# Kernel tuning notes

Measured on AMD Instinct MI355X. Metric: run time of the kernel, lower is better.

Reference implementation:

```python
import jax, jax.numpy as jnp
import numpy as np

WAY, SHOT, P, FDIM, HDIM, NHEADS = 5, 5, 10, 640, 512, 8
H = W = 14
NUM_SPT = WAY * SHOT
EPS_BN = 1e-5
EPS_LN = 1e-5


def _l2norm(x, axis=-1):
    n = jnp.linalg.norm(x, axis=axis, keepdims=True)
    return x / jnp.maximum(n, 1e-12)


def _cbr(x, Wc, bc, g, beta):
    # 1x1 conv + BatchNorm(train stats) + ReLU. x: [N,C,H,W], Wc: [O,C]
    y = jnp.einsum('nchw,oc->nohw', x, Wc) + bc[None, :, None, None]
    mu = y.mean((0, 2, 3))
    var = y.var((0, 2, 3))
    y = (y - mu[None, :, None, None]) / jnp.sqrt(var[None, :, None, None] + EPS_BN)
    y = y * g[None, :, None, None] + beta[None, :, None, None]
    return jax.nn.relu(y)


def _mha(x, Wq, bq, Wk, bk, Wv, bv, Wa, ba, ln_g, ln_b):
    B, S, D = x.shape
    dk = D // NHEADS
    def proj(Wt, bt):
        return (x @ Wt.T + bt).reshape(B, S, NHEADS, dk).transpose(0, 2, 1, 3)
    q, k, v = proj(Wq, bq), proj(Wk, bk), proj(Wv, bv)
    scores = jnp.einsum('bhqd,bhkd->bhqk', q, k) / jnp.sqrt(jnp.asarray(dk, x.dtype))
    att = jax.nn.softmax(scores, axis=-1)
    ctx = jnp.einsum('bhqk,bhkd->bhqd', att, v).transpose(0, 2, 1, 3).reshape(B, S, D)
    out = ctx @ Wa.T + ba + x  # residual
    mu = out.mean(-1, keepdims=True)
    var = out.var(-1, keepdims=True)
    return ((out - mu) / jnp.sqrt(var + EPS_LN)) * ln_g + ln_b


def setup_inputs() -> dict:
    k = jax.random.key(0)
    ks = jax.random.split(k, 16)
    s = 0.02
    return {
        'key':   jax.random.normal(ks[0], (NUM_SPT + 75, FDIM, H, W), jnp.float32),
        'query': jax.random.normal(ks[1], (75, FDIM, H, W), jnp.float32),
        'Wc':  jax.random.normal(ks[2], (HDIM, FDIM), jnp.float32) * s,
        'bc':  jnp.zeros((HDIM,), jnp.float32),
        'g1':  jnp.ones((HDIM,), jnp.float32),
        'b1':  jnp.zeros((HDIM,), jnp.float32),
        'Wq':  jax.random.normal(ks[3], (HDIM, HDIM), jnp.float32) * s,
        'bq':  jnp.zeros((HDIM,), jnp.float32),
        'Wk':  jax.random.normal(ks[4], (HDIM, HDIM), jnp.float32) * s,
        'bk':  jnp.zeros((HDIM,), jnp.float32),
        'Wv':  jax.random.normal(ks[5], (HDIM, HDIM), jnp.float32) * s,
        'bv':  jnp.zeros((HDIM,), jnp.float32),
        'Wa':  jax.random.normal(ks[6], (HDIM, HDIM), jnp.float32) * s,
        'ba':  jnp.zeros((HDIM,), jnp.float32),
        'ln_g': jnp.ones((HDIM,), jnp.float32),
        'ln_b': jnp.zeros((HDIM,), jnp.float32),
        'Wm':  jax.random.normal(ks[7], (P, HDIM), jnp.float32) * s,
        'Wo':  jax.random.normal(ks[8], (FDIM, HDIM), jnp.float32) * s,
        'bo':  jnp.zeros((FDIM,), jnp.float32),
        'g2':  jnp.ones((FDIM,), jnp.float32),
        'b2':  jnp.zeros((FDIM,), jnp.float32),
    }


def reference(key, query, Wc, bc, g1, b1, Wq, bq, Wk, bk, Wv, bv, Wa, ba, ln_g, ln_b, Wm, Wo, bo, g2, b2):
    # proto_concept: conv1x1 + BN + ReLU
    key_ = _cbr(key, Wc, bc, g1, b1)                 # [B, HDIM, H, W]
    B, D, h, w = key_.shape
    feats = key_.transpose(0, 2, 3, 1).reshape(B, h * w, D)
    support = feats[:NUM_SPT].reshape(SHOT, WAY, h * w, D).mean(0)   # [WAY, hw, D]
    qf = feats[NUM_SPT:]                                             # [NQ, hw, D]
    nq = B - NUM_SPT

    support = _mha(support, Wq, bq, Wk, bk, Wv, bv, Wa, ba, ln_g, ln_b)
    qf = _mha(qf, Wq, bq, Wk, bk, Wv, bv, Wa, ba, ln_g, ln_b)

    # prototype formation: softmax over all support positions (dim 0)
    mw = (support @ Wm.T).reshape(-1, P, 1)          # [WAY*hw, P, 1]
    mw = jax.nn.softmax(mw, axis=0)
    sflat = support.reshape(-1, D)                   # [WAY*hw, D]
    protos = (mw * sflat[:, None, :]).sum(0)         # [P, D]

    # ---- query_loss (training branch) ----
    protos_n = _l2norm(protos)                       # [P, D]

    # diversity loss (faithful to original incl. triu over (P, D) dims)
    diff2 = (protos_n[None, :, :] - protos_n[:, None, :]) ** 2   # [P, P, D]
    dis = 1.0 - diff2[None]                                      # [1, P, P, D]
    dis = dis * (dis > 0).astype(dis.dtype)
    tri = jnp.triu(jnp.ones((P, D), dis.dtype), k=1)
    dis = dis * tri
    dis_loss = (dis.sum(1).sum(1) * 2.0 / (P * (P - 1))).mean()

    cst_loss = ((protos_n[1:] - protos_n[:-1]) ** 2).sum(-1).mean()

    # dual-softmax scoring (protos shared across batch)
    score = jnp.einsum('bnd,md->bnm', qf, protos_n)  # [NQ, hw, P]
    sp = jax.nn.softmax(score, axis=-1)
    new_q = _l2norm(jnp.einsum('bnm,md->bnd', sp, protos_n))

    idx = jnp.argmax(score, axis=-1)                 # top-1 proto per position
    pos = protos_n[idx]                              # [NQ, hw, D]
    fea_loss = jnp.mean((qf - pos) ** 2)

    uq = new_q.transpose(0, 2, 1).reshape(nq, D, h, w)
    updated = _cbr(uq, Wo, bo, g2, b2) + query       # [NQ, FDIM, H, W]
    return (updated, fea_loss, cst_loss, dis_loss)
```

## Files before the change

kernel.cpp:

```cpp
#include <hip/hip_runtime.h>
#include <math.h>

#define WAYS 5
#define SHOTS 5
#define PP 10
#define FDIMC 640
#define HD 512
#define SEQ 196
#define NB 100
#define NQB 75
#define NMHA 80
#define M1 (NB*SEQ)
#define MMHA (NMHA*SEQ)
#define MQ (NQB*SEQ)
#define NBLK_ROWK (MQ/4)
#define OUT_UPD (NQB*FDIMC*SEQ)

#define OFF_CS1S 0
#define OFF_CS1Q 512
#define OFF_CS2S 1024
#define OFF_CS2Q 1664
#define ZERO_FLOATS 2306
#define OFF_ST1SC 2308
#define OFF_ST1SH 2820
#define OFF_ST2SC 3332
#define OFF_ST2SH 3972
#define OFF_M    4612
#define OFF_PN   14412

#define RB 20480
#define RC (RB + 15439360)
#define RD (RC + 8028160)
#define RE (RD + 8028160)
#define RF (RE + 8028160)
#define RG (RF + 4014080)
#define RH (RG + 4014080)
#define OFF_FEAP (RF + 3763200)
#define OFF_WSM  RB
#define OFF_PPART (RB + 16384)

typedef __bf16 bf16x8 __attribute__((ext_vector_type(8)));
typedef float f32x4 __attribute__((ext_vector_type(4)));

__device__ __forceinline__ ushort f2bf(float f) {
  unsigned u = __float_as_uint(f);
  return (ushort)((u + 0x7fffu + ((u >> 16) & 1u)) >> 16);
}

__device__ __forceinline__ f32x4 mfma16(bf16x8 a, bf16x8 b, f32x4 c) {
  return __builtin_amdgcn_mfma_f32_16x16x32_bf16(a, b, c, 0, 0, 0);
}

__device__ __forceinline__ float waveSum(float v) {
#pragma unroll
  for (int o = 32; o; o >>= 1) v += __shfl_xor(v, o, 64);
  return v;
}


__global__ __launch_bounds__(256) void key_transpose(const float* __restrict__ key,
                                                     ushort* __restrict__ keyT) {
  __shared__ float T[32][33];
  const int n = blockIdx.z, c0 = blockIdx.y*32, s0 = blockIdx.x*32;
  const int tj = threadIdx.x & 31, ti = threadIdx.x >> 5;
#pragma unroll
  for (int it = 0; it < 4; ++it) {
    const int cl = it*8 + ti;
    const int s = s0 + tj;
    T[cl][tj] = (s < SEQ) ? key[((size_t)n*FDIMC + c0 + cl)*SEQ + s] : 0.f;
  }
  __syncthreads();
#pragma unroll
  for (int it = 0; it < 4; ++it) {
    const int sl = it*8 + ti;
    const int s = s0 + sl;
    if (s < SEQ) keyT[((size_t)(n*SEQ + s))*FDIMC + c0 + tj] = f2bf(T[tj][sl]);
  }
}

__global__ void wconvert(const float* __restrict__ Wc, const float* __restrict__ Wq,
                         const float* __restrict__ Wk, const float* __restrict__ Wv,
                         const float* __restrict__ Wa, const float* __restrict__ Wo,
                         ushort* __restrict__ wh) {
  const int i = blockIdx.x*256 + threadIdx.x;
  float v;
  if (i < 327680) v = Wc[i];
  else if (i < 589824) v = Wq[i - 327680];
  else if (i < 851968) v = Wk[i - 589824];
  else if (i < 1114112) v = Wv[i - 851968];
  else if (i < 1376256) v = Wa[i - 1114112];
  else v = Wo[i - 1376256];
  wh[i] = f2bf(v);
}

template<int OM, int CS>
__global__ __launch_bounds__(256) void gemm_bf(const ushort* __restrict__ A,
    const ushort* __restrict__ W, const float* __restrict__ bias,
    float* __restrict__ Cf, ushort* __restrict__ Ch, int M, int N, int K,
    float* __restrict__ gsum, float* __restrict__ gsq) {
  __shared__ ushort As[128*32];
  __shared__ ushort Bs[128*32];
  __shared__ float csum[128], csq[128];
  const int tid = threadIdx.x;
  const int m0 = blockIdx.y*128, n0 = blockIdx.x*128;
  const int w = tid >> 6, lane = tid & 63;
  const int wr = w >> 1, wc = w & 1;
  const int g = lane >> 4, c = lane & 15;

  const int ch0 = tid, ch1 = 256 + tid;
  const int ar0 = ch0 >> 2, ar1 = ch1 >> 2;
  const int ak0 = (ch0 & 3) * 8, ak1 = (ch1 & 3) * 8;
  int gr0 = m0 + ar0; if (gr0 > M-1) gr0 = M-1;
  int gr1 = m0 + ar1; if (gr1 > M-1) gr1 = M-1;
  const ushort* Ap0 = A + (size_t)gr0*K + ak0;
  const ushort* Ap1 = A + (size_t)gr1*K + ak1;
  const ushort* Wp0 = W + (size_t)(n0 + ar0)*K + ak0;
  const ushort* Wp1 = W + (size_t)(n0 + ar1)*K + ak1;

  f32x4 acc[4][4];
#pragma unroll
  for (int i = 0; i < 4; ++i)
#pragma unroll
    for (int j = 0; j < 4; ++j) acc[i][j] = (f32x4)(0.0f);

  for (int k0 = 0; k0 < K; k0 += 32) {
    const uint4 a0 = *(const uint4*)(Ap0 + k0);
    const uint4 a1 = *(const uint4*)(Ap1 + k0);
    const uint4 b0 = *(const uint4*)(Wp0 + k0);
    const uint4 b1 = *(const uint4*)(Wp1 + k0);
    __syncthreads();
    *(uint4*)(&As[ch0*8]) = a0;
    *(uint4*)(&As[ch1*8]) = a1;
    *(uint4*)(&Bs[ch0*8]) = b0;
    *(uint4*)(&Bs[ch1*8]) = b1;
    __syncthreads();
    bf16x8 af[4], bfr[4];
#pragma unroll
    for (int mi = 0; mi < 4; ++mi)
      af[mi] = *(const bf16x8*)(&As[(wr*64 + mi*16 + c)*32 + g*8]);
#pragma unroll
    for (int ni = 0; ni < 4; ++ni)
      bfr[ni] = *(const bf16x8*)(&Bs[(wc*64 + ni*16 + c)*32 + g*8]);
#pragma unroll
    for (int mi = 0; mi < 4; ++mi)
#pragma unroll
      for (int ni = 0; ni < 4; ++ni)
        acc[mi][ni] = mfma16(af[mi], bfr[ni], acc[mi][ni]);
  }

  if (CS) {
    __syncthreads();
    if (tid < 128) { csum[tid] = 0.f; csq[tid] = 0.f; }
    __syncthreads();
  }

#pragma unroll
  for (int ni = 0; ni < 4; ++ni) {
    const int col = n0 + wc*64 + ni*16 + c;
    const float bb = bias[col];
    float ls = 0.f, lq = 0.f;
#pragma unroll
    for (int mi = 0; mi < 4; ++mi) {
#pragma unroll
      for (int q = 0; q < 4; ++q) {
        const int row = m0 + wr*64 + mi*16 + g*4 + q;
        if (row < M) {
          const float v = acc[mi][ni][q] + bb;
          if (OM == 0) Cf[(size_t)row*N + col] = v;
          else if (OM == 1) Ch[(size_t)row*N + col] = f2bf(v);
          else Ch[(size_t)row*N + col] = f2bf(v*0.125f);
          if (CS) { ls += v; lq += v*v; }
        }
      }
    }
    if (CS) {
      const int lcol = wc*64 + ni*16 + c;
      atomicAdd(&csum[lcol], ls);
      atomicAdd(&csq[lcol], lq);
    }
  }
  if (CS) {
    __syncthreads();
    if (tid < 128) {
      atomicAdd(&gsum[n0 + tid], csum[tid]);
      atomicAdd(&gsq[n0 + tid], csq[tid]);
    }
  }
}


__global__ void bn_finalize(const float* __restrict__ sums, const float* __restrict__ sumsq,
    const float* __restrict__ g, const float* __restrict__ b, int C, float invM,
    float* __restrict__ scale, float* __restrict__ shift) {
  const int c = blockIdx.x*256 + threadIdx.x;
  if (c >= C) return;
  const float mu = sums[c]*invM;
  const float var = sumsq[c]*invM - mu*mu;
  const float sc = rsqrtf(var + 1e-5f) * g[c];
  scale[c] = sc;
  shift[c] = b[c] - mu*sc;
}

__global__ __launch_bounds__(256) void bn1_apply(const float* __restrict__ y1,
    const float* __restrict__ scale, const float* __restrict__ shift,
    float* __restrict__ sraw, float* __restrict__ xbuf, ushort* __restrict__ xbufh) {
  const int i4 = blockIdx.x*256 + threadIdx.x;
  if (i4 >= M1*HD/4) return;
  const int e = i4 << 2;
  const int col = e & (HD - 1);
  float4 v = ((const float4*)y1)[i4];
  v.x = fmaxf(fmaf(v.x, scale[col],   shift[col]),   0.f);
  v.y = fmaxf(fmaf(v.y, scale[col+1], shift[col+1]), 0.f);
  v.z = fmaxf(fmaf(v.z, scale[col+2], shift[col+2]), 0.f);
  v.w = fmaxf(fmaf(v.w, scale[col+3], shift[col+3]), 0.f);
  if (e < 25*SEQ*HD) ((float4*)sraw)[i4] = v;
  else {
    const int o4 = i4 - (20*SEQ*HD/4);
    ((float4*)xbuf)[o4] = v;
    ushort4 hv = make_ushort4(f2bf(v.x), f2bf(v.y), f2bf(v.z), f2bf(v.w));
    *(ushort4*)(xbufh + (size_t)o4*4) = hv;
  }
}

__global__ void support_mean(const float* __restrict__ sraw, float* __restrict__ xbuf,
                             ushort* __restrict__ xbufh) {
  const int i4 = blockIdx.x*256 + threadIdx.x;
  if (i4 >= WAYS*SEQ*HD/4) return;
  const int e = i4 << 2;
  const int w = e / (SEQ*HD);
  const int rem = e - w*(SEQ*HD);
  float4 acc = make_float4(0.f,0.f,0.f,0.f);
#pragma unroll
  for (int s = 0; s < SHOTS; ++s) {
    const float4 v = *(const float4*)(sraw + (s*WAYS + w)*(SEQ*HD) + rem);
    acc.x += v.x; acc.y += v.y; acc.z += v.z; acc.w += v.w;
  }
  acc.x *= 0.2f; acc.y *= 0.2f; acc.z *= 0.2f; acc.w *= 0.2f;
  ((float4*)xbuf)[i4] = acc;
  ushort4 hv = make_ushort4(f2bf(acc.x), f2bf(acc.y), f2bf(acc.z), f2bf(acc.w));
  *(ushort4*)(xbufh + (size_t)i4*4) = hv;
}


__global__ __launch_bounds__(256) void attn_qk(const ushort* __restrict__ qb,
    const ushort* __restrict__ kb, ushort* __restrict__ P) {
  __shared__ ushort Ks[208*72];
  const int bh = blockIdx.x, b = bh >> 3, h = bh & 7;
  const int tid = threadIdx.x;
  for (int idx = tid; idx < 208*8; idx += 256) {
    const int row = idx >> 3, part = idx & 7;
    uint4 v = make_uint4(0u,0u,0u,0u);
    if (row < SEQ) v = *(const uint4*)(kb + ((size_t)(b*SEQ + row))*HD + h*64 + part*8);
    *(uint4*)(&Ks[row*72 + part*8]) = v;
  }
  __syncthreads();
  const int w = tid >> 6, lane = tid & 63, g = lane >> 4, c = lane & 15;
  for (int rt = w; rt < 13; rt += 4) {
    int qrow = b*SEQ + rt*16 + c; if (qrow > MMHA-1) qrow = MMHA-1;
    const bf16x8 aq0 = *(const bf16x8*)(qb + (size_t)qrow*HD + h*64 + g*8);
    const bf16x8 aq1 = *(const bf16x8*)(qb + (size_t)qrow*HD + h*64 + 32 + g*8);
    f32x4 acc[13];
#pragma unroll
    for (int ct = 0; ct < 13; ++ct) acc[ct] = (f32x4)(0.0f);
#pragma unroll
    for (int ct = 0; ct < 13; ++ct) {
      const bf16x8 b0 = *(const bf16x8*)(&Ks[(ct*16 + c)*72 + g*8]);
      const bf16x8 b1 = *(const bf16x8*)(&Ks[(ct*16 + c)*72 + 32 + g*8]);
      acc[ct] = mfma16(aq0, b0, acc[ct]);
      acc[ct] = mfma16(aq1, b1, acc[ct]);
    }
    if (c >= 4) acc[12] = (f32x4)(-1e30f);
    float mrow[4], Z[4];
#pragma unroll
    for (int q = 0; q < 4; ++q) {
      float mx = acc[0][q];
#pragma unroll
      for (int ct = 1; ct < 13; ++ct) mx = fmaxf(mx, acc[ct][q]);
      mrow[q] = mx;
    }
#pragma unroll
    for (int q = 0; q < 4; ++q) {
#pragma unroll
      for (int msk = 1; msk < 16; msk <<= 1)
        mrow[q] = fmaxf(mrow[q], __shfl_xor(mrow[q], msk, 64));
    }
#pragma unroll
    for (int q = 0; q < 4; ++q) Z[q] = 0.f;
#pragma unroll
    for (int ct = 0; ct < 13; ++ct)
#pragma unroll
      for (int q = 0; q < 4; ++q) {
        const float e = __expf(acc[ct][q] - mrow[q]);
        acc[ct][q] = e; Z[q] += e;
      }
#pragma unroll
    for (int q = 0; q < 4; ++q) {
#pragma unroll
      for (int msk = 1; msk < 16; msk <<= 1) Z[q] += __shfl_xor(Z[q], msk, 64);
      Z[q] = 1.f / Z[q];
    }
    const size_t pb = (size_t)bh*(208*232);
#pragma unroll
    for (int q = 0; q < 4; ++q) {
      ushort* pr = P + pb + (size_t)(rt*16 + g*4 + q)*232;
#pragma unroll
      for (int ct = 0; ct < 13; ++ct) pr[ct*16 + c] = f2bf(acc[ct][q]*Z[q]);
      pr[208 + c] = 0;
      if (c < 8) pr[224 + c] = 0;
    }
  }
}


__global__ __launch_bounds__(256) void v_transpose(const ushort* __restrict__ vb,
                                                   ushort* __restrict__ VT) {
  __shared__ ushort Vs[196*72];
  const int bh = blockIdx.x, b = bh >> 3, h = bh & 7;
  const int tid = threadIdx.x;
  for (int idx = tid; idx < 196*8; idx += 256) {
    const int row = idx >> 3, part = idx & 7;
    *(uint4*)(&Vs[row*72 + part*8]) =
        *(const uint4*)(vb + ((size_t)(b*SEQ + row))*HD + h*64 + part*8);
  }
  __syncthreads();
  ushort* o = VT + (size_t)bh*64*224;
  for (int idx = tid; idx < 64*224; idx += 256) {
    const int d = idx/224, s = idx - d*224;
    o[idx] = (s < SEQ) ? Vs[s*72 + d] : (ushort)0;
  }
}


__global__ __launch_bounds__(256) void attn_pv(const ushort* __restrict__ P,
    const ushort* __restrict__ VT, ushort* __restrict__ ctx) {
  __shared__ ushort Ps[112*232];
  const int bh = blockIdx.x, b = bh >> 3, h = bh & 7;
  const int tid = threadIdx.x, w = tid >> 6, lane = tid & 63, g = lane >> 4, c = lane & 15;
  bf16x8 bv[7];
  const ushort* vt = VT + (size_t)bh*64*224 + (size_t)(w*16 + c)*224;
#pragma unroll
  for (int ks = 0; ks < 7; ++ks) bv[ks] = *(const bf16x8*)(vt + ks*32 + g*8);
  const char* pg = (const char*)(P + (size_t)bh*(208*232));
#pragma unroll
  for (int half = 0; half < 2; ++half) {
    const int r0 = half ? 112 : 0;
    const int nbytes = half ? 96*464 : 112*464;
    __syncthreads();
    for (int byte = tid*16; byte < nbytes; byte += 4096)
      *(uint4*)((char*)Ps + byte) = *(const uint4*)(pg + r0*464 + byte);
    __syncthreads();
    const int rtlo = half ? 7 : 0, rthi = half ? 13 : 7;
    for (int rt = rtlo; rt < rthi; ++rt) {
      const int lrow = rt*16 - r0 + c;
      f32x4 acc = (f32x4)(0.0f);
#pragma unroll
      for (int ks = 0; ks < 7; ++ks) {
        const bf16x8 a = *(const bf16x8*)(&Ps[lrow*232 + ks*32 + g*8]);
        acc = mfma16(a, bv[ks], acc);
      }
#pragma unroll
      for (int q = 0; q < 4; ++q) {
        const int srow = rt*16 + g*4 + q;
        if (srow < SEQ)
          ctx[((size_t)(b*SEQ + srow))*HD + h*64 + w*16 + c] = f2bf(acc[q]);
      }
    }
  }
}


__global__ __launch_bounds__(256) void ln_kernel(const float* __restrict__ tmp,
    const float* __restrict__ xin, const float* __restrict__ g,
    const float* __restrict__ bta, float* __restrict__ out) {
  const int row = blockIdx.x*4 + (threadIdx.x >> 6);
  const int lane = threadIdx.x & 63;
  const float* t = tmp + (size_t)row*HD;
  const float* x = xin + (size_t)row*HD;
  float v[8]; float s = 0.f;
#pragma unroll
  for (int i = 0; i < 8; ++i) { const float val = t[i*64 + lane] + x[i*64 + lane]; v[i] = val; s += val; }
  s = waveSum(s);
  const float mu = s * (1.f/HD);
  float sq = 0.f;
#pragma unroll
  for (int i = 0; i < 8; ++i) { const float d = v[i] - mu; sq += d*d; }
  sq = waveSum(sq);
  const float istd = rsqrtf(sq*(1.f/HD) + 1e-5f);
#pragma unroll
  for (int i = 0; i < 8; ++i) {
    const int d = i*64 + lane;
    out[(size_t)row*HD + d] = (v[i] - mu)*istd*g[d] + bta[d];
  }
}


__global__ __launch_bounds__(256) void mw_kernel(const float* __restrict__ xout,
    const float* __restrict__ Wm, float* __restrict__ m) {
  const int row = blockIdx.x*4 + (threadIdx.x >> 6);
  const int lane = threadIdx.x & 63;
  const float* x = xout + (size_t)row*HD;
  float xv[8];
#pragma unroll
  for (int i = 0; i < 8; ++i) xv[i] = x[i*64 + lane];
#pragma unroll
  for (int p = 0; p < PP; ++p) {
    const float* wp = Wm + p*HD;
    float s = 0.f;
#pragma unroll
    for (int i = 0; i < 8; ++i) s = fmaf(xv[i], wp[i*64 + lane], s);
    s = waveSum(s);
    if (lane == 0) m[row*PP + p] = s;
  }
}

__global__ __launch_bounds__(256) void wsm_kernel(const float* __restrict__ m,
                                                  float* __restrict__ wsm) {
  __shared__ float red[256];
  const int p = blockIdx.x, tid = threadIdx.x;
  float lmax = -1e30f;
  for (int r = tid; r < 980; r += 256) lmax = fmaxf(lmax, m[r*PP + p]);
  red[tid] = lmax; __syncthreads();
  for (int s = 128; s; s >>= 1) { if (tid < s) red[tid] = fmaxf(red[tid], red[tid+s]); __syncthreads(); }
  const float bmax = red[0]; __syncthreads();
  float lsum = 0.f;
  for (int r = tid; r < 980; r += 256) {
    const float e = __expf(m[r*PP + p] - bmax);
    wsm[p*980 + r] = e; lsum += e;
  }
  red[tid] = lsum; __syncthreads();
  for (int s = 128; s; s >>= 1) { if (tid < s) red[tid] += red[tid+s]; __syncthreads(); }
  const float invZ = 1.f / red[0];
  for (int r = tid; r < 980; r += 256) wsm[p*980 + r] *= invZ;
}

__global__ __launch_bounds__(256) void protos_part(const float* __restrict__ wsm,
    const float* __restrict__ xout, float* __restrict__ part) {
  const int p = blockIdx.y, chunk = blockIdx.x, tid = threadIdx.x;
  const int r0 = chunk*49;
  float a0 = 0.f, a1 = 0.f;
  for (int r = r0; r < r0 + 49; ++r) {
    const float w = wsm[p*980 + r];
    a0 = fmaf(w, xout[(size_t)r*HD + tid], a0);
    a1 = fmaf(w, xout[(size_t)r*HD + tid + 256], a1);
  }
  float* o = part + (((size_t)p*20 + chunk) << 9);
  o[tid] = a0;
  o[tid + 256] = a1;
}

__global__ __launch_bounds__(256) void protos_fin(const float* __restrict__ part,
                                                  float* __restrict__ pn) {
  __shared__ float red[256];
  const int p = blockIdx.x, tid = threadIdx.x;
  float a0 = 0.f, a1 = 0.f;
  for (int cch = 0; cch < 20; ++cch) {
    const float* o = part + (((size_t)p*20 + cch) << 9);
    a0 += o[tid];
    a1 += o[tid + 256];
  }
  red[tid] = a0*a0 + a1*a1; __syncthreads();
  for (int s = 128; s; s >>= 1) { if (tid < s) red[tid] += red[tid+s]; __syncthreads(); }
  const float rn = 1.f / fmaxf(sqrtf(red[0]), 1e-12f);
  pn[p*HD + tid] = a0*rn;
  pn[p*HD + tid + 256] = a1*rn;
}

__global__ __launch_bounds__(256) void losses_kernel(const float* __restrict__ pn, float* __restrict__ out) {
  __shared__ float redc[256], redd[256];
  const int tid = threadIdx.x;
  float cpart = 0.f, dpart = 0.f;
  for (int d = tid; d < HD; d += 256) {
    float a[PP];
#pragma unroll
    for (int j = 0; j < PP; ++j) a[j] = pn[j*HD + d];
#pragma unroll
    for (int j = 0; j < PP; ++j) {
      if (d > j) {
#pragma unroll
        for (int i = 0; i < PP; ++i) {
          const float df = a[j] - a[i];
          const float t = 1.f - df*df;
          if (t > 0.f) dpart += t;
        }
      }
    }
#pragma unroll
    for (int j = 0; j < PP - 1; ++j) { const float df = a[j+1] - a[j]; cpart += df*df; }
  }
  redc[tid] = cpart; redd[tid] = dpart; __syncthreads();
  for (int s = 128; s; s >>= 1) {
    if (tid < s) { redc[tid] += redc[tid+s]; redd[tid] += redd[tid+s]; }
    __syncthreads();
  }
  if (tid == 0) {
    out[OUT_UPD + 1] = redc[0] / 9.f;
    out[OUT_UPD + 2] = redd[0] * (2.f / (90.f * 512.f));
  }
}

__global__ __launch_bounds__(256) void rowk(const float* __restrict__ xout, const float* __restrict__ pn,
    ushort* __restrict__ newq, float* __restrict__ feapart) {
  __shared__ float Ps[PP*HD];
  __shared__ float fred[4];
  const int tid = threadIdx.x;
  for (int idx = tid; idx < PP*HD; idx += 256) Ps[idx] = pn[idx];
  __syncthreads();
  const int row = blockIdx.x*4 + (tid >> 6);
  const int lane = tid & 63;
  const float* x = xout + (size_t)(WAYS*SEQ + row)*HD;
  float xv[8];
#pragma unroll
  for (int i = 0; i < 8; ++i) xv[i] = x[i*64 + lane];
  float sc[PP];
#pragma unroll
  for (int p = 0; p < PP; ++p) {
    float s = 0.f;
#pragma unroll
    for (int i = 0; i < 8; ++i) s = fmaf(xv[i], Ps[p*HD + i*64 + lane], s);
    sc[p] = waveSum(s);
  }
  float mx = sc[0]; int am = 0;
#pragma unroll
  for (int p = 1; p < PP; ++p) if (sc[p] > mx) { mx = sc[p]; am = p; }
  float Z = 0.f; float sp[PP];
#pragma unroll
  for (int p = 0; p < PP; ++p) { const float e = expf(sc[p] - mx); sp[p] = e; Z += e; }
  const float rz = 1.f / Z;
  float nv[8]; float ss = 0.f;
#pragma unroll
  for (int i = 0; i < 8; ++i) {
    float a = 0.f;
#pragma unroll
    for (int p = 0; p < PP; ++p) a = fmaf(sp[p], Ps[p*HD + i*64 + lane], a);
    a *= rz; nv[i] = a; ss += a*a;
  }
  ss = waveSum(ss);
  const float rn = 1.f / fmaxf(sqrtf(ss), 1e-12f);
#pragma unroll
  for (int i = 0; i < 8; ++i) newq[(size_t)row*HD + i*64 + lane] = f2bf(nv[i]*rn);
  float fp = 0.f;
#pragma unroll
  for (int i = 0; i < 8; ++i) { const float d = xv[i] - Ps[am*HD + i*64 + lane]; fp += d*d; }
  fp = waveSum(fp);
  if (lane == 0) fred[tid >> 6] = fp;
  __syncthreads();
  if (tid == 0) feapart[blockIdx.x] = fred[0] + fred[1] + fred[2] + fred[3];
}

__global__ __launch_bounds__(256) void fea_finalize(const float* __restrict__ feapart,
                                                    float* __restrict__ out) {
  __shared__ float red[256];
  float s = 0.f;
  for (int i = threadIdx.x; i < NBLK_ROWK; i += 256) s += feapart[i];
  red[threadIdx.x] = s; __syncthreads();
  for (int st = 128; st; st >>= 1) {
    if (threadIdx.x < st) red[threadIdx.x] += red[threadIdx.x + st];
    __syncthreads();
  }
  if (threadIdx.x == 0) out[OUT_UPD] = red[0] / (float)((size_t)NQB*SEQ*HD);
}

__global__ __launch_bounds__(256) void bn2_apply(const float* __restrict__ y2, const float* __restrict__ scale,
    const float* __restrict__ shift, const float* __restrict__ query, float* __restrict__ out) {
  __shared__ float tile[32][33];
  const int n = blockIdx.z, o0 = blockIdx.y*32, hw0 = blockIdx.x*32;
  const int tj = threadIdx.x & 31, ti = threadIdx.x >> 5;
#pragma unroll
  for (int it = 0; it < 4; ++it) {
    const int hw = hw0 + it*8 + ti;
    const int o = o0 + tj;
    float v = 0.f;
    if (hw < SEQ) v = fmaxf(fmaf(y2[((size_t)n*SEQ + hw)*FDIMC + o], scale[o], shift[o]), 0.f);
    tile[it*8 + ti][tj] = v;
  }
  __syncthreads();
#pragma unroll
  for (int it = 0; it < 4; ++it) {
    const int o = o0 + it*8 + ti;
    const int hw = hw0 + tj;
    if (hw < SEQ) {
      const size_t oi = ((size_t)n*FDIMC + o)*SEQ + hw;
      out[oi] = tile[tj][it*8 + ti] + query[oi];
    }
  }
}

extern "C" void kernel_launch(void* const* d_in, const int* in_sizes, int n_in,
                              void* d_out, int out_size, void* d_ws, size_t ws_size,
                              hipStream_t stream) {
  const float* key   = (const float*)d_in[0];
  const float* query = (const float*)d_in[1];
  const float* Wc    = (const float*)d_in[2];
  const float* bc    = (const float*)d_in[3];
  const float* g1    = (const float*)d_in[4];
  const float* b1    = (const float*)d_in[5];
  const float* Wq    = (const float*)d_in[6];
  const float* bq    = (const float*)d_in[7];
  const float* Wk    = (const float*)d_in[8];
  const float* bk    = (const float*)d_in[9];
  const float* Wv    = (const float*)d_in[10];
  const float* bv    = (const float*)d_in[11];
  const float* Wa    = (const float*)d_in[12];
  const float* ba    = (const float*)d_in[13];
  const float* ln_g  = (const float*)d_in[14];
  const float* ln_b  = (const float*)d_in[15];
  const float* Wm    = (const float*)d_in[16];
  const float* Wo    = (const float*)d_in[17];
  const float* bo    = (const float*)d_in[18];
  const float* g2    = (const float*)d_in[19];
  const float* b2    = (const float*)d_in[20];
  float* out = (float*)d_out;
  float* w = (float*)d_ws;

  float*  y1    = w + RB;
  ushort* P     = (ushort*)(w + RB);
  float*  y2    = w + RB;
  float*  xbuf  = w + RC;
  ushort* keyT  = (ushort*)(w + RD);
  ushort* qb    = (ushort*)(w + RD);
  float*  tmp   = w + RD;
  ushort* xbufh = (ushort*)(w + RE);
  ushort* VT    = (ushort*)(w + RE);
  float*  xout  = w + RE;
  float*  sraw  = w + RF;
  ushort* kb    = (ushort*)(w + RF);
  ushort* newq  = (ushort*)(w + RF);
  ushort* vb    = (ushort*)(w + RG);
  ushort* ctx   = (ushort*)(w + RG);
  ushort* wh    = (ushort*)(w + RH);
  float*  feapart = w + OFF_FEAP;
  float*  wsm   = w + OFF_WSM;
  float*  ppart = w + OFF_PPART;
  ushort* Wcb = wh;
  ushort* Wqb = wh + 327680;
  ushort* Wkb = wh + 589824;
  ushort* Wvb = wh + 851968;
  ushort* Wab = wh + 1114112;
  ushort* Wob = wh + 1376256;

  hipMemsetAsync(w, 0, ZERO_FLOATS*sizeof(float), stream);

  key_transpose<<<dim3(7, 20, NB), 256, 0, stream>>>(key, keyT);
  wconvert<<<6656, 256, 0, stream>>>(Wc, Wq, Wk, Wv, Wa, Wo, wh);

  gemm_bf<0,1><<<dim3(4, 154), 256, 0, stream>>>(keyT, Wcb, bc, y1, nullptr, M1, HD, FDIMC,
                                                 w + OFF_CS1S, w + OFF_CS1Q);
  bn_finalize<<<2, 256, 0, stream>>>(w + OFF_CS1S, w + OFF_CS1Q, g1, b1, HD, 1.f/M1,
                                     w + OFF_ST1SC, w + OFF_ST1SH);
  bn1_apply<<<M1*HD/4/256, 256, 0, stream>>>(y1, w + OFF_ST1SC, w + OFF_ST1SH, sraw, xbuf, xbufh);
  support_mean<<<WAYS*SEQ*HD/4/256, 256, 0, stream>>>(sraw, xbuf, xbufh);

  gemm_bf<2,0><<<dim3(4, 123), 256, 0, stream>>>(xbufh, Wqb, bq, nullptr, qb, MMHA, HD, HD, nullptr, nullptr);
  gemm_bf<1,0><<<dim3(4, 123), 256, 0, stream>>>(xbufh, Wkb, bk, nullptr, kb, MMHA, HD, HD, nullptr, nullptr);
  gemm_bf<1,0><<<dim3(4, 123), 256, 0, stream>>>(xbufh, Wvb, bv, nullptr, vb, MMHA, HD, HD, nullptr, nullptr);

  v_transpose<<<NMHA*8, 256, 0, stream>>>(vb, VT);
  attn_qk<<<NMHA*8, 256, 0, stream>>>(qb, kb, P);
  attn_pv<<<NMHA*8, 256, 0, stream>>>(P, VT, ctx);

  gemm_bf<0,0><<<dim3(4, 123), 256, 0, stream>>>(ctx, Wab, ba, tmp, nullptr, MMHA, HD, HD, nullptr, nullptr);
  ln_kernel<<<MMHA/4, 256, 0, stream>>>(tmp, xbuf, ln_g, ln_b, xout);

  mw_kernel<<<245, 256, 0, stream>>>(xout, Wm, w + OFF_M);
  wsm_kernel<<<PP, 256, 0, stream>>>(w + OFF_M, wsm);
  protos_part<<<dim3(20, PP), 256, 0, stream>>>(wsm, xout, ppart);
  protos_fin<<<PP, 256, 0, stream>>>(ppart, w + OFF_PN);
  losses_kernel<<<1, 256, 0, stream>>>(w + OFF_PN, out);
  rowk<<<NBLK_ROWK, 256, 0, stream>>>(xout, w + OFF_PN, newq, feapart);

  gemm_bf<0,1><<<dim3(5, 115), 256, 0, stream>>>(newq, Wob, bo, y2, nullptr, MQ, FDIMC, HD,
                                                 w + OFF_CS2S, w + OFF_CS2Q);
  bn_finalize<<<3, 256, 0, stream>>>(w + OFF_CS2S, w + OFF_CS2Q, g2, b2, FDIMC, 1.f/MQ,
                                     w + OFF_ST2SC, w + OFF_ST2SH);
  fea_finalize<<<1, 256, 0, stream>>>(feapart, out);
  bn2_apply<<<dim3(7, 20, NQB), 256, 0, stream>>>(y2, w + OFF_ST2SC, w + OFF_ST2SH, query, out);
}
```

Before: 393.0 us.

## Store conv1 output and intermediate activations in bf16 instead of fp32

The first conv GEMM now writes bf16, and bn1_apply, support_mean, ln_kernel and the downstream proto/rowk kernels read and write bf16 activations instead of fp32 copies. The fp32 xbuf/sraw/xout buffers are dropped, and workspace regions are remapped so the new buffers do not collide. This roughly halves the memory traffic of these bandwidth-bound elementwise kernels. In exchange it adds bf16 rounding to the residual input of the layer norm and to the proto computation.

```diff
diff --git a/kernel.cpp b/kernel.cpp
--- a/kernel.cpp
+++ b/kernel.cpp
@@ -35,9 +35,10 @@
 #define RF (RE + 8028160)
 #define RG (RF + 4014080)
 #define RH (RG + 4014080)
+#define OFF_XOUT (RB + 10000000)
 #define OFF_FEAP (RF + 3763200)
-#define OFF_WSM  RB
-#define OFF_PPART (RB + 16384)
+#define OFF_WSM  RG
+#define OFF_PPART (RG + 16384)
 
 typedef __bf16 bf16x8 __attribute__((ext_vector_type(8)));
 typedef float f32x4 __attribute__((ext_vector_type(4)));
@@ -45,6 +46,9 @@
 __device__ __forceinline__ ushort f2bf(float f) {
   unsigned u = __float_as_uint(f);
   return (ushort)((u + 0x7fffu + ((u >> 16) & 1u)) >> 16);
+}
+__device__ __forceinline__ float bf2f(ushort u) {
+  return __uint_as_float(((unsigned)u) << 16);
 }
 
 __device__ __forceinline__ f32x4 mfma16(bf16x8 a, bf16x8 b, f32x4 c) {
@@ -201,44 +205,51 @@
   shift[c] = b[c] - mu*sc;
 }
 
-__global__ __launch_bounds__(256) void bn1_apply(const float* __restrict__ y1,
+__global__ __launch_bounds__(256) void bn1_apply(const ushort* __restrict__ y1,
     const float* __restrict__ scale, const float* __restrict__ shift,
-    float* __restrict__ sraw, float* __restrict__ xbuf, ushort* __restrict__ xbufh) {
-  const int i4 = blockIdx.x*256 + threadIdx.x;
-  if (i4 >= M1*HD/4) return;
-  const int e = i4 << 2;
+    ushort* __restrict__ srawh, ushort* __restrict__ xbufh) {
+  const int i8 = blockIdx.x*256 + threadIdx.x;
+  if (i8 >= M1*HD/8) return;
+  const int e = i8 << 3;
   const int col = e & (HD - 1);
-  float4 v = ((const float4*)y1)[i4];
-  v.x = fmaxf(fmaf(v.x, scale[col],   shift[col]),   0.f);
-  v.y = fmaxf(fmaf(v.y, scale[col+1], shift[col+1]), 0.f);
-  v.z = fmaxf(fmaf(v.z, scale[col+2], shift[col+2]), 0.f);
-  v.w = fmaxf(fmaf(v.w, scale[col+3], shift[col+3]), 0.f);
-  if (e < 25*SEQ*HD) ((float4*)sraw)[i4] = v;
-  else {
-    const int o4 = i4 - (20*SEQ*HD/4);
-    ((float4*)xbuf)[o4] = v;
-    ushort4 hv = make_ushort4(f2bf(v.x), f2bf(v.y), f2bf(v.z), f2bf(v.w));
-    *(ushort4*)(xbufh + (size_t)o4*4) = hv;
-  }
-}
-
-__global__ void support_mean(const float* __restrict__ sraw, float* __restrict__ xbuf,
-                             ushort* __restrict__ xbufh) {
-  const int i4 = blockIdx.x*256 + threadIdx.x;
-  if (i4 >= WAYS*SEQ*HD/4) return;
-  const int e = i4 << 2;
+  const uint4 raw = ((const uint4*)y1)[i8];
+  unsigned rw[4] = {raw.x, raw.y, raw.z, raw.w};
+  unsigned res[4];
+#pragma unroll
+  for (int j = 0; j < 4; ++j) {
+    float v0 = bf2f((ushort)(rw[j] & 0xffffu));
+    float v1 = bf2f((ushort)(rw[j] >> 16));
+    v0 = fmaxf(fmaf(v0, scale[col + 2*j],     shift[col + 2*j]),     0.f);
+    v1 = fmaxf(fmaf(v1, scale[col + 2*j + 1], shift[col + 2*j + 1]), 0.f);
+    res[j] = (unsigned)f2bf(v0) | ((unsigned)f2bf(v1) << 16);
+  }
+  const uint4 o = make_uint4(res[0], res[1], res[2], res[3]);
+  if (e < 25*SEQ*HD) ((uint4*)srawh)[i8] = o;
+  else ((uint4*)xbufh)[i8 - (20*SEQ*HD/8)] = o;
+}
+
+__global__ void support_mean(const ushort* __restrict__ srawh, ushort* __restrict__ xbufh) {
+  const int i8 = blockIdx.x*256 + threadIdx.x;
+  if (i8 >= WAYS*SEQ*HD/8) return;
+  const int e = i8 << 3;
   const int w = e / (SEQ*HD);
   const int rem = e - w*(SEQ*HD);
-  float4 acc = make_float4(0.f,0.f,0.f,0.f);
+  float acc[8] = {};
 #pragma unroll
   for (int s = 0; s < SHOTS; ++s) {
-    const float4 v = *(const float4*)(sraw + (s*WAYS + w)*(SEQ*HD) + rem);
-    acc.x += v.x; acc.y += v.y; acc.z += v.z; acc.w += v.w;
-  }
-  acc.x *= 0.2f; acc.y *= 0.2f; acc.z *= 0.2f; acc.w *= 0.2f;
-  ((float4*)xbuf)[i4] = acc;
-  ushort4 hv = make_ushort4(f2bf(acc.x), f2bf(acc.y), f2bf(acc.z), f2bf(acc.w));
-  *(ushort4*)(xbufh + (size_t)i4*4) = hv;
+    const uint4 v = *(const uint4*)(srawh + (size_t)(s*WAYS + w)*(SEQ*HD) + rem);
+    const unsigned rw[4] = {v.x, v.y, v.z, v.w};
+#pragma unroll
+    for (int j = 0; j < 4; ++j) {
+      acc[2*j]   += bf2f((ushort)(rw[j] & 0xffffu));
+      acc[2*j+1] += bf2f((ushort)(rw[j] >> 16));
+    }
+  }
+  unsigned res[4];
+#pragma unroll
+  for (int j = 0; j < 4; ++j)
+    res[j] = (unsigned)f2bf(acc[2*j]*0.2f) | ((unsigned)f2bf(acc[2*j+1]*0.2f) << 16);
+  ((uint4*)xbufh)[i8] = make_uint4(res[0], res[1], res[2], res[3]);
 }
 
 
@@ -370,15 +381,18 @@
 
 
 __global__ __launch_bounds__(256) void ln_kernel(const float* __restrict__ tmp,
-    const float* __restrict__ xin, const float* __restrict__ g,
-    const float* __restrict__ bta, float* __restrict__ out) {
+    const ushort* __restrict__ xin, const float* __restrict__ g,
+    const float* __restrict__ bta, ushort* __restrict__ outh) {
   const int row = blockIdx.x*4 + (threadIdx.x >> 6);
   const int lane = threadIdx.x & 63;
   const float* t = tmp + (size_t)row*HD;
-  const float* x = xin + (size_t)row*HD;
+  const ushort* x = xin + (size_t)row*HD;
   float v[8]; float s = 0.f;
 #pragma unroll
-  for (int i = 0; i < 8; ++i) { const float val = t[i*64 + lane] + x[i*64 + lane]; v[i] = val; s += val; }
+  for (int i = 0; i < 8; ++i) {
+    const float val = t[i*64 + lane] + bf2f(x[i*64 + lane]);
+    v[i] = val; s += val;
+  }
   s = waveSum(s);
   const float mu = s * (1.f/HD);
   float sq = 0.f;
@@ -389,19 +403,19 @@
 #pragma unroll
   for (int i = 0; i < 8; ++i) {
     const int d = i*64 + lane;
-    out[(size_t)row*HD + d] = (v[i] - mu)*istd*g[d] + bta[d];
-  }
-}
-
-
-__global__ __launch_bounds__(256) void mw_kernel(const float* __restrict__ xout,
+    outh[(size_t)row*HD + d] = f2bf((v[i] - mu)*istd*g[d] + bta[d]);
+  }
+}
+
+
+__global__ __launch_bounds__(256) void mw_kernel(const ushort* __restrict__ xout,
     const float* __restrict__ Wm, float* __restrict__ m) {
   const int row = blockIdx.x*4 + (threadIdx.x >> 6);
   const int lane = threadIdx.x & 63;
-  const float* x = xout + (size_t)row*HD;
+  const ushort* x = xout + (size_t)row*HD;
   float xv[8];
 #pragma unroll
-  for (int i = 0; i < 8; ++i) xv[i] = x[i*64 + lane];
+  for (int i = 0; i < 8; ++i) xv[i] = bf2f(x[i*64 + lane]);
 #pragma unroll
   for (int p = 0; p < PP; ++p) {
     const float* wp = Wm + p*HD;
@@ -434,14 +448,14 @@
 }
 
 __global__ __launch_bounds__(256) void protos_part(const float* __restrict__ wsm,
-    const float* __restrict__ xout, float* __restrict__ part) {
+    const ushort* __restrict__ xout, float* __restrict__ part) {
   const int p = blockIdx.y, chunk = blockIdx.x, tid = threadIdx.x;
   const int r0 = chunk*49;
   float a0 = 0.f, a1 = 0.f;
   for (int r = r0; r < r0 + 49; ++r) {
     const float w = wsm[p*980 + r];
-    a0 = fmaf(w, xout[(size_t)r*HD + tid], a0);
-    a1 = fmaf(w, xout[(size_t)r*HD + tid + 256], a1);
+    a0 = fmaf(w, bf2f(xout[(size_t)r*HD + tid]), a0);
+    a1 = fmaf(w, bf2f(xout[(size_t)r*HD + tid + 256]), a1);
   }
   float* o = part + (((size_t)p*20 + chunk) << 9);
   o[tid] = a0;
@@ -498,7 +512,7 @@
   }
 }
 
-__global__ __launch_bounds__(256) void rowk(const float* __restrict__ xout, const float* __restrict__ pn,
+__global__ __launch_bounds__(256) void rowk(const ushort* __restrict__ xout, const float* __restrict__ pn,
     ushort* __restrict__ newq, float* __restrict__ feapart) {
   __shared__ float Ps[PP*HD];
   __shared__ float fred[4];
@@ -507,10 +521,10 @@
   __syncthreads();
   const int row = blockIdx.x*4 + (tid >> 6);
   const int lane = tid & 63;
-  const float* x = xout + (size_t)(WAYS*SEQ + row)*HD;
+  const ushort* x = xout + (size_t)(WAYS*SEQ + row)*HD;
   float xv[8];
 #pragma unroll
-  for (int i = 0; i < 8; ++i) xv[i] = x[i*64 + lane];
+  for (int i = 0; i < 8; ++i) xv[i] = bf2f(x[i*64 + lane]);
   float sc[PP];
 #pragma unroll
   for (int p = 0; p < PP; ++p) {
@@ -612,17 +626,16 @@
   float* out = (float*)d_out;
   float* w = (float*)d_ws;
 
-  float*  y1    = w + RB;
+  ushort* y1h   = (ushort*)(w + RB);
   ushort* P     = (ushort*)(w + RB);
-  float*  y2    = w + RB;
-  float*  xbuf  = w + RC;
+  float*  y2f   = w + RB;
+  ushort* xouth = (ushort*)(w + OFF_XOUT);
+  ushort* VT    = (ushort*)(w + RC);
   ushort* keyT  = (ushort*)(w + RD);
   ushort* qb    = (ushort*)(w + RD);
-  float*  tmp   = w + RD;
+  float*  tmpf  = w + RD;
   ushort* xbufh = (ushort*)(w + RE);
-  ushort* VT    = (ushort*)(w + RE);
-  float*  xout  = w + RE;
-  float*  sraw  = w + RF;
+  ushort* srawh = (ushort*)(w + RF);
   ushort* kb    = (ushort*)(w + RF);
   ushort* newq  = (ushort*)(w + RF);
   ushort* vb    = (ushort*)(w + RG);
@@ -643,12 +656,12 @@
   key_transpose<<<dim3(7, 20, NB), 256, 0, stream>>>(key, keyT);
   wconvert<<<6656, 256, 0, stream>>>(Wc, Wq, Wk, Wv, Wa, Wo, wh);
 
-  gemm_bf<0,1><<<dim3(4, 154), 256, 0, stream>>>(keyT, Wcb, bc, y1, nullptr, M1, HD, FDIMC,
+  gemm_bf<1,1><<<dim3(4, 154), 256, 0, stream>>>(keyT, Wcb, bc, nullptr, y1h, M1, HD, FDIMC,
                                                  w + OFF_CS1S, w + OFF_CS1Q);
   bn_finalize<<<2, 256, 0, stream>>>(w + OFF_CS1S, w + OFF_CS1Q, g1, b1, HD, 1.f/M1,
                                      w + OFF_ST1SC, w + OFF_ST1SH);
-  bn1_apply<<<M1*HD/4/256, 256, 0, stream>>>(y1, w + OFF_ST1SC, w + OFF_ST1SH, sraw, xbuf, xbufh);
-  support_mean<<<WAYS*SEQ*HD/4/256, 256, 0, stream>>>(sraw, xbuf, xbufh);
+  bn1_apply<<<M1*HD/8/256, 256, 0, stream>>>(y1h, w + OFF_ST1SC, w + OFF_ST1SH, srawh, xbufh);
+  support_mean<<<WAYS*SEQ*HD/8/256, 256, 0, stream>>>(srawh, xbufh);
 
   gemm_bf<2,0><<<dim3(4, 123), 256, 0, stream>>>(xbufh, Wqb, bq, nullptr, qb, MMHA, HD, HD, nullptr, nullptr);
   gemm_bf<1,0><<<dim3(4, 123), 256, 0, stream>>>(xbufh, Wkb, bk, nullptr, kb, MMHA, HD, HD, nullptr, nullptr);
@@ -658,20 +671,20 @@
   attn_qk<<<NMHA*8, 256, 0, stream>>>(qb, kb, P);
   attn_pv<<<NMHA*8, 256, 0, stream>>>(P, VT, ctx);
 
-  gemm_bf<0,0><<<dim3(4, 123), 256, 0, stream>>>(ctx, Wab, ba, tmp, nullptr, MMHA, HD, HD, nullptr, nullptr);
-  ln_kernel<<<MMHA/4, 256, 0, stream>>>(tmp, xbuf, ln_g, ln_b, xout);
-
-  mw_kernel<<<245, 256, 0, stream>>>(xout, Wm, w + OFF_M);
+  gemm_bf<0,0><<<dim3(4, 123), 256, 0, stream>>>(ctx, Wab, ba, tmpf, nullptr, MMHA, HD, HD, nullptr, nullptr);
+  ln_kernel<<<MMHA/4, 256, 0, stream>>>(tmpf, xbufh, ln_g, ln_b, xouth);
+
+  mw_kernel<<<245, 256, 0, stream>>>(xouth, Wm, w + OFF_M);
   wsm_kernel<<<PP, 256, 0, stream>>>(w + OFF_M, wsm);
-  protos_part<<<dim3(20, PP), 256, 0, stream>>>(wsm, xout, ppart);
+  protos_part<<<dim3(20, PP), 256, 0, stream>>>(wsm, xouth, ppart);
   protos_fin<<<PP, 256, 0, stream>>>(ppart, w + OFF_PN);
   losses_kernel<<<1, 256, 0, stream>>>(w + OFF_PN, out);
-  rowk<<<NBLK_ROWK, 256, 0, stream>>>(xout, w + OFF_PN, newq, feapart);
-
-  gemm_bf<0,1><<<dim3(5, 115), 256, 0, stream>>>(newq, Wob, bo, y2, nullptr, MQ, FDIMC, HD,
+  rowk<<<NBLK_ROWK, 256, 0, stream>>>(xouth, w + OFF_PN, newq, feapart);
+
+  gemm_bf<0,1><<<dim3(5, 115), 256, 0, stream>>>(newq, Wob, bo, y2f, nullptr, MQ, FDIMC, HD,
                                                  w + OFF_CS2S, w + OFF_CS2Q);
   bn_finalize<<<3, 256, 0, stream>>>(w + OFF_CS2S, w + OFF_CS2Q, g2, b2, FDIMC, 1.f/MQ,
                                      w + OFF_ST2SC, w + OFF_ST2SH);
   fea_finalize<<<1, 256, 0, stream>>>(feapart, out);
-  bn2_apply<<<dim3(7, 20, NQB), 256, 0, stream>>>(y2, w + OFF_ST2SC, w + OFF_ST2SH, query, out);
-}
+  bn2_apply<<<dim3(7, 20, NQB), 256, 0, stream>>>(y2f, w + OFF_ST2SC, w + OFF_ST2SH, query, out);
+}
```

After: 381.0 us. 1.03x faster.
